# Optimization experiments

Hardware: AMD Instinct MI355X
Metric: run time of the kernel (lower is better)

The kernel has to match this reference:

```python
import jax, jax.numpy as jnp
import numpy as np

N, E, D, ED, SH = 100000, 1600000, 64, 16, 9

# Real spherical harmonics l=0,1,2, 'integral' normalization (e3nn default),
# applied to unit direction vectors. Coefficients: 1/(2*sqrt(pi)), sqrt(3/4pi), etc.

def _sh(d):
    x, y, z = d[:, 0], d[:, 1], d[:, 2]
    return jnp.stack([
        jnp.full_like(x, 0.28209479177387814),          # l=0
        0.4886025119029199 * y,                          # l=1, m=-1
        0.4886025119029199 * z,                          # l=1, m=0
        0.4886025119029199 * x,                          # l=1, m=1
        1.0925484305920792 * x * y,                      # l=2, m=-2
        1.0925484305920792 * y * z,                      # l=2, m=-1
        0.31539156525252005 * (3.0 * z * z - 1.0),       # l=2, m=0
        1.0925484305920792 * x * z,                      # l=2, m=1
        0.5462742152960396 * (x * x - y * y),            # l=2, m=2
    ], axis=1)


def _mlp(h, W1, b1, W2, b2):  # Linear -> SiLU -> Linear
    return jax.nn.silu(h @ W1 + b1) @ W2 + b2


def setup_inputs() -> dict:
    key = jax.random.key(0)
    ks = jax.random.split(key, 16)
    def rn(k, shape, scale=0.05):
        return jax.random.normal(k, shape, dtype=jnp.float32) * scale
    return {
        "x": jax.random.normal(ks[0], (N, D), jnp.float32),
        "pos": jax.random.normal(ks[1], (N, 3), jnp.float32) * 3.0,
        "edge_attr": jax.random.normal(ks[2], (E, ED), jnp.float32),
        "row": jax.random.randint(ks[3], (E,), 0, N, dtype=jnp.int32),
        "col": jax.random.randint(ks[4], (E,), 0, N, dtype=jnp.int32),
        "node_W1": rn(ks[5], (D, D)), "node_b1": jnp.zeros((D,), jnp.float32),
        "node_W2": rn(ks[6], (D, D)), "node_b2": jnp.zeros((D,), jnp.float32),
        "edge_W1": rn(ks[7], (SH + ED, D)), "edge_b1": jnp.zeros((D,), jnp.float32),
        "edge_W2": rn(ks[8], (D, D)), "edge_b2": jnp.zeros((D,), jnp.float32),
        "out_W1": rn(ks[9], (2 * D, D)), "out_b1": jnp.zeros((D,), jnp.float32),
        "out_W2": rn(ks[10], (D, D)), "out_b2": jnp.zeros((D,), jnp.float32),
        "bn_gamma": jnp.ones((D,), jnp.float32), "bn_beta": jnp.zeros((D,), jnp.float32),
    }


def reference(x, pos, edge_attr, row, col,
              node_W1, node_b1, node_W2, node_b2,
              edge_W1, edge_b1, edge_W2, edge_b2,
              out_W1, out_b1, out_W2, out_b2,
              bn_gamma, bn_beta):
    # gather node positions per edge -> relative vectors
    rel = pos[row] - pos[col]                                    # [E,3]
    length = jnp.sqrt(jnp.sum(rel * rel, axis=1, keepdims=True) + 1e-12)
    d = rel / length
    d = d / (jnp.sqrt(jnp.sum(d * d, axis=1, keepdims=True)) + 1e-10)
    edge_sh = _sh(d)                                             # [E,9]
    edge_feat = jnp.concatenate([edge_sh, edge_attr], axis=1)    # [E,9+ED]
    x_t = _mlp(x, node_W1, node_b1, node_W2, node_b2)            # [N,D]
    e_w = _mlp(edge_feat, edge_W1, edge_b1, edge_W2, edge_b2)    # [E,D]
    msg = x_t[row] * e_w                                         # message = x_j * edge_attr
    # scatter-mean onto target nodes (edge_index[1] == col)
    s = jax.ops.segment_sum(msg, col, num_segments=N)            # [N,D]
    cnt = jax.ops.segment_sum(jnp.ones((E,), msg.dtype), col, num_segments=N)
    agg = s / jnp.maximum(cnt, 1.0)[:, None]
    h = jnp.concatenate([agg, x], axis=1)                        # [N,2D]
    h = _mlp(h, out_W1, out_b1, out_W2, out_b2)                  # [N,D]
    # BatchNorm over node dim (scalar irreps), training-mode batch stats
    mean = jnp.mean(h, axis=0)
    var = jnp.var(h, axis=0)
    return (h - mean) / jnp.sqrt(var + 1e-5) * bn_gamma + bn_beta
```

## Files before the change

kernel.cpp:

```cpp
#include <hip/hip_runtime.h>
#include <math.h>

#define DD 64
#define EDA 16

#define FR_E1 0
#define FR_E2 4
#define FR_N1 12
#define FR_N2 20
#define FR_O1 28
#define FR_O2 44
#define FR_TOT 52

#define PADH 72
#define PADF 68

#define HS 72
#define PF 68

typedef unsigned int u32;
typedef __attribute__((ext_vector_type(8))) short short8;
typedef __attribute__((ext_vector_type(4))) float f32x4;

static __device__ __forceinline__ float silu(float v) {
    return v / (1.0f + __expf(-v));
}
static __device__ __forceinline__ unsigned short f2bf(float f) {
    unsigned u = __float_as_uint(f);
    unsigned r = u + 0x7FFFu + ((u >> 16) & 1u);
    return (unsigned short)(r >> 16);
}
static __device__ __forceinline__ float bf2f(unsigned short u) {
    return __uint_as_float(((unsigned)u) << 16);
}
static __device__ __forceinline__ unsigned cvt_pk_bf16(float lo, float hi) {
    unsigned r;
    asm("v_cvt_pk_bf16_f32 %0, %1, %2" : "=v"(r) : "v"(lo), "v"(hi));
    return r;
}
static __device__ __forceinline__ int bperm(int idx_lane, int v) {
    return __builtin_amdgcn_ds_bpermute(idx_lane << 2, v);
}
static __device__ __forceinline__ void wave_lds_fence() {
    asm volatile("s_waitcnt lgkmcnt(0)" ::: "memory");
    __builtin_amdgcn_sched_barrier(0);
}

__global__ __launch_bounds__(256) void k_pack_w(
    const float* __restrict__ eW1, const float* __restrict__ eW2,
    const float* __restrict__ nW1, const float* __restrict__ nW2,
    const float* __restrict__ oW1, const float* __restrict__ oW2,
    unsigned short* __restrict__ wpk)
{
    int t = threadIdx.x;
    int nt = t >> 6, l = t & 63;
    int kc = l >> 4, n0 = l & 15;

    #pragma unroll
    for (int j = 0; j < 8; ++j) {
        int k = kc*8 + j;
        int orig = (k < 16) ? (9 + k) : ((k < 25) ? (k - 16) : -1);
        float v = (orig >= 0) ? eW1[orig*DD + nt*16 + n0] : 0.0f;
        wpk[((size_t)((FR_E1 + nt)*64 + l))*8 + j] = f2bf(v);
    }
    #pragma unroll
    for (int s = 0; s < 2; ++s) {
        #pragma unroll
        for (int j = 0; j < 8; ++j) {
            int k = s*32 + kc*8 + j;
            wpk[((size_t)((FR_E2 + s*4 + nt)*64 + l))*8 + j] = f2bf(eW2[k*DD + nt*16 + n0]);
            wpk[((size_t)((FR_N1 + s*4 + nt)*64 + l))*8 + j] = f2bf(nW1[k*DD + nt*16 + n0]);
            wpk[((size_t)((FR_N2 + s*4 + nt)*64 + l))*8 + j] = f2bf(nW2[k*DD + nt*16 + n0]);
            wpk[((size_t)((FR_O2 + s*4 + nt)*64 + l))*8 + j] = f2bf(oW2[k*DD + nt*16 + n0]);
        }
    }
    #pragma unroll
    for (int s = 0; s < 4; ++s) {
        #pragma unroll
        for (int j = 0; j < 8; ++j) {
            int k = s*32 + kc*8 + j;
            wpk[((size_t)((FR_O1 + s*4 + nt)*64 + l))*8 + j] = f2bf(oW1[k*DD + nt*16 + n0]);
        }
    }
}

__global__ __launch_bounds__(256) void k_hist(
    const int* __restrict__ col, u32* __restrict__ cnt, int n_e)
{
    int g = blockIdx.x * 256 + threadIdx.x;
    int base = g * 4;
    if (base + 3 < n_e) {
        int4 c = ((const int4*)col)[g];
        atomicAdd(&cnt[c.x], 1u);
        atomicAdd(&cnt[c.y], 1u);
        atomicAdd(&cnt[c.z], 1u);
        atomicAdd(&cnt[c.w], 1u);
    } else {
        for (int e = base; e < n_e; ++e) atomicAdd(&cnt[col[e]], 1u);
    }
}

__global__ __launch_bounds__(256) void k_scan1(
    const u32* __restrict__ cnt, u32* __restrict__ bsum, int n)
{
    __shared__ u32 s[256];
    int i = blockIdx.x * 256 + threadIdx.x;
    s[threadIdx.x] = (i < n) ? cnt[i] : 0u;
    __syncthreads();
    for (int o = 128; o > 0; o >>= 1) {
        if (threadIdx.x < o) s[threadIdx.x] += s[threadIdx.x + o];
        __syncthreads();
    }
    if (threadIdx.x == 0) bsum[blockIdx.x] = s[0];
}

__global__ __launch_bounds__(512) void k_scan2(
    const u32* __restrict__ bsum, u32* __restrict__ boff, int nb)
{
    __shared__ u32 s[512];
    int t = threadIdx.x;
    u32 v = (t < nb) ? bsum[t] : 0u;
    s[t] = v;
    __syncthreads();
    for (int o = 1; o < 512; o <<= 1) {
        u32 a = (t >= o) ? s[t - o] : 0u;
        __syncthreads();
        s[t] += a;
        __syncthreads();
    }
    if (t < nb) boff[t] = s[t] - v;
}

__global__ __launch_bounds__(256) void k_scan3(
    const u32* __restrict__ cnt, const u32* __restrict__ boff,
    u32* __restrict__ wp, int n)
{
    __shared__ u32 s[256];
    int t = threadIdx.x;
    int i = blockIdx.x * 256 + t;
    u32 v = (i < n) ? cnt[i] : 0u;
    s[t] = v;
    __syncthreads();
    for (int o = 1; o < 256; o <<= 1) {
        u32 a = (t >= o) ? s[t - o] : 0u;
        __syncthreads();
        s[t] += a;
        __syncthreads();
    }
    if (i < n) wp[i] = boff[blockIdx.x] + s[t] - v;
}

__global__ __launch_bounds__(256) void k_scatter(
    const int* __restrict__ row, const int* __restrict__ col,
    u32* __restrict__ wp, uint2* __restrict__ ce, int n_e)
{
    int e = blockIdx.x * 256 + threadIdx.x;
    if (e >= n_e) return;
    int c = col[e];
    int r = row[e];
    u32 p = atomicAdd(&wp[c], 1u);
    uint2 pk;
    pk.x = (u32)e | ((u32)r << 21);
    pk.y = ((u32)r >> 11) | ((u32)c << 6);
    ce[p] = pk;
}

__global__ __launch_bounds__(256, 2) void k_node_mfma(
    const float* __restrict__ x,
    const unsigned short* __restrict__ wpk,
    const float* __restrict__ b1, const float* __restrict__ b2,
    unsigned short* __restrict__ x_tb, int n)
{
    __shared__ __align__(16) unsigned short tile[4][16*PADH];
    const int tid  = threadIdx.x;
    const int wv   = tid >> 6;
    const int lane = tid & 63;
    const int kc   = lane >> 4;
    const int n0   = lane & 15;
    const int rbase = kc * 4;

    const short8* fb = (const short8*)wpk;
    short8 bw1[2][4], bw2[2][4];
    #pragma unroll
    for (int s = 0; s < 2; ++s)
        #pragma unroll
        for (int nt = 0; nt < 4; ++nt) {
            bw1[s][nt] = fb[(FR_N1 + s*4 + nt)*64 + lane];
            bw2[s][nt] = fb[(FR_N2 + s*4 + nt)*64 + lane];
        }
    float b1v[4], b2v[4];
    #pragma unroll
    for (int nt = 0; nt < 4; ++nt) { b1v[nt] = b1[nt*16 + n0]; b2v[nt] = b2[nt*16 + n0]; }

    const int base = blockIdx.x*64 + wv*16;
    int rc = min(base + n0, n - 1);
    const float* xr = x + (size_t)rc * DD;

    short8 a[2];
    #pragma unroll
    for (int m = 0; m < 2; ++m) {
        float4 u0 = *(const float4*)(xr + m*32 + kc*8);
        float4 u1 = *(const float4*)(xr + m*32 + kc*8 + 4);
        unsigned* au = (unsigned*)&a[m];
        au[0] = cvt_pk_bf16(u0.x, u0.y);
        au[1] = cvt_pk_bf16(u0.z, u0.w);
        au[2] = cvt_pk_bf16(u1.x, u1.y);
        au[3] = cvt_pk_bf16(u1.z, u1.w);
    }

    f32x4 zz = {0.f, 0.f, 0.f, 0.f};
    f32x4 hacc[4] = {zz, zz, zz, zz};
    #pragma unroll
    for (int m = 0; m < 2; ++m)
        #pragma unroll
        for (int nt = 0; nt < 4; ++nt)
            hacc[nt] = __builtin_amdgcn_mfma_f32_16x16x32_bf16(a[m], bw1[m][nt], hacc[nt], 0, 0, 0);

    #pragma unroll
    for (int nt = 0; nt < 4; ++nt)
        #pragma unroll
        for (int r = 0; r < 4; ++r)
            tile[wv][(rbase + r)*PADH + nt*16 + n0] = f2bf(silu(hacc[nt][r] + b1v[nt]));
    __syncthreads();

    short8 a2_0 = *(const short8*)&tile[wv][n0*PADH +  0 + kc*8];
    short8 a2_1 = *(const short8*)&tile[wv][n0*PADH + 32 + kc*8];
    f32x4 oacc[4];
    #pragma unroll
    for (int nt = 0; nt < 4; ++nt) {
        oacc[nt] = __builtin_amdgcn_mfma_f32_16x16x32_bf16(a2_0, bw2[0][nt], zz, 0, 0, 0);
        oacc[nt] = __builtin_amdgcn_mfma_f32_16x16x32_bf16(a2_1, bw2[1][nt], oacc[nt], 0, 0, 0);
    }
    __syncthreads();

    #pragma unroll
    for (int nt = 0; nt < 4; ++nt)
        #pragma unroll
        for (int r = 0; r < 4; ++r)
            tile[wv][(rbase + r)*PADH + nt*16 + n0] = f2bf(oacc[nt][r] + b2v[nt]);
    __syncthreads();

    int ei = lane >> 2, q = lane & 3;
    int er = base + ei;
    if (er < n) {
        uint4* dst = (uint4*)(x_tb + (size_t)er * DD);
        dst[q]     = *(const uint4*)&tile[wv][ei*PADH + q*8];
        dst[q + 4] = *(const uint4*)&tile[wv][ei*PADH + (q + 4)*8];
    }
}

__global__ __launch_bounds__(256, 3) void k_edge_fused(
    const float* __restrict__ pos,
    const float* __restrict__ edge_attr,
    const uint2* __restrict__ ce,
    const unsigned short* __restrict__ x_tb,
    const unsigned short* __restrict__ wpk,
    const float* __restrict__ b1, const float* __restrict__ b2,
    float* __restrict__ agg, int n_e)
{
    __shared__ __align__(16) unsigned short hid_s[4][16*HS];
    __shared__ __align__(16) float          msg_s[4][16*PF];

    const int tid  = threadIdx.x;
    const int wv   = tid >> 6;
    const int lane = tid & 63;
    const int kc   = lane >> 4;
    const int n0   = lane & 15;

    const short8* fb = (const short8*)wpk;
    short8 bw1[4], bw2[2][4];
    #pragma unroll
    for (int nt = 0; nt < 4; ++nt) bw1[nt] = fb[(FR_E1 + nt)*64 + lane];
    #pragma unroll
    for (int s = 0; s < 2; ++s)
        #pragma unroll
        for (int nt = 0; nt < 4; ++nt) bw2[s][nt] = fb[(FR_E2 + s*4 + nt)*64 + lane];

    float4 b1q[4], b2q[4];
    #pragma unroll
    for (int nt = 0; nt < 4; ++nt) {
        b1q[nt] = *(const float4*)(b1 + nt*16 + kc*4);
        b2q[nt] = *(const float4*)(b2 + nt*16 + kc*4);
    }

    const int gbase = blockIdx.x*256 + wv*64;
    int g  = gbase + lane;
    int gc = min(g, n_e - 1);
    uint2 pk = ce[gc];
    int eo = (int)(pk.x & 0x1FFFFFu);
    int rw = (int)((pk.x >> 21) | ((pk.y & 0x3Fu) << 11));
    int cl = (int)(pk.y >> 6);

    float ax = pos[3*rw+0] - pos[3*cl+0];
    float ay = pos[3*rw+1] - pos[3*cl+1];
    float az = pos[3*rw+2] - pos[3*cl+2];
    float len = sqrtf(fmaf(ax,ax, fmaf(ay,ay, az*az)) + 1e-12f);
    float dx = ax/len, dy = ay/len, dz = az/len;
    float n2 = sqrtf(fmaf(dx,dx, fmaf(dy,dy, dz*dz)));
    float inv = 1.0f/(n2 + 1e-10f);
    dx *= inv; dy *= inv; dz *= inv;

    u32 shp01 = cvt_pk_bf16(0.28209479177387814f, 0.4886025119029199f*dy);
    u32 shp23 = cvt_pk_bf16(0.4886025119029199f*dz, 0.4886025119029199f*dx);
    u32 shp45 = cvt_pk_bf16(1.0925484305920792f*dx*dy, 1.0925484305920792f*dy*dz);
    u32 shp67 = cvt_pk_bf16(0.31539156525252005f*(3.0f*dz*dz - 1.0f),
                            1.0925484305920792f*dx*dz);
    u32 shp8  = cvt_pk_bf16(0.5462742152960396f*(dx*dx - dy*dy), 0.0f);

    f32x4 zz = {0.f, 0.f, 0.f, 0.f};

    #pragma unroll 1
    for (int t = 0; t < 4; ++t) {
        const int le = t*16 + n0;
        bool valid = (gbase + le) < n_e;

        int ea  = bperm(le, eo);
        int rv  = bperm(le, rw);
        u32 s01 = (u32)bperm(le, (int)shp01);
        u32 s23 = (u32)bperm(le, (int)shp23);
        u32 s45 = (u32)bperm(le, (int)shp45);
        u32 s67 = (u32)bperm(le, (int)shp67);
        u32 s8  = (u32)bperm(le, (int)shp8);

        const unsigned short* xrow = x_tb + (size_t)rv * DD;
        uint2 xv0 = *(const uint2*)(xrow +  0 + kc*4);
        uint2 xv1 = *(const uint2*)(xrow + 16 + kc*4);
        uint2 xv2 = *(const uint2*)(xrow + 32 + kc*4);
        uint2 xv3 = *(const uint2*)(xrow + 48 + kc*4);
        if (!valid) {
            xv0.x = xv0.y = xv1.x = xv1.y = 0u;
            xv2.x = xv2.y = xv3.x = xv3.y = 0u;
        }

        short8 af;
        unsigned* au = (unsigned*)&af;
        if (kc < 2) {
            const float4* ap = (const float4*)(edge_attr + (size_t)ea*EDA + kc*8);
            float4 a0 = ap[0], a1 = ap[1];
            au[0] = cvt_pk_bf16(a0.x, a0.y);
            au[1] = cvt_pk_bf16(a0.z, a0.w);
            au[2] = cvt_pk_bf16(a1.x, a1.y);
            au[3] = cvt_pk_bf16(a1.z, a1.w);
        } else if (kc == 2) {
            au[0] = s01; au[1] = s23; au[2] = s45; au[3] = s67;
        } else {
            au[0] = s8; au[1] = 0u; au[2] = 0u; au[3] = 0u;
        }

        f32x4 hacc[4];
        #pragma unroll
        for (int nt = 0; nt < 4; ++nt)
            hacc[nt] = __builtin_amdgcn_mfma_f32_16x16x32_bf16(bw1[nt], af, zz, 0, 0, 0);

        #pragma unroll
        for (int nt = 0; nt < 4; ++nt) {
            float h0 = silu(hacc[nt][0] + b1q[nt].x);
            float h1 = silu(hacc[nt][1] + b1q[nt].y);
            float h2 = silu(hacc[nt][2] + b1q[nt].z);
            float h3 = silu(hacc[nt][3] + b1q[nt].w);
            uint2 pr;
            pr.x = cvt_pk_bf16(h0, h1);
            pr.y = cvt_pk_bf16(h2, h3);
            *(uint2*)&hid_s[wv][n0*HS + nt*16 + kc*4] = pr;
        }
        wave_lds_fence();

        short8 bf0 = *(const short8*)&hid_s[wv][n0*HS +  0 + kc*8];
        short8 bf1 = *(const short8*)&hid_s[wv][n0*HS + 32 + kc*8];
        f32x4 oacc[4];
        #pragma unroll
        for (int nt = 0; nt < 4; ++nt) {
            oacc[nt] = __builtin_amdgcn_mfma_f32_16x16x32_bf16(bw2[0][nt], bf0, zz, 0, 0, 0);
            oacc[nt] = __builtin_amdgcn_mfma_f32_16x16x32_bf16(bw2[1][nt], bf1, oacc[nt], 0, 0, 0);
        }

        {
            float4 m;
            m.x = (oacc[0][0] + b2q[0].x) * bf2f((unsigned short)(xv0.x));
            m.y = (oacc[0][1] + b2q[0].y) * bf2f((unsigned short)(xv0.x >> 16));
            m.z = (oacc[0][2] + b2q[0].z) * bf2f((unsigned short)(xv0.y));
            m.w = (oacc[0][3] + b2q[0].w) * bf2f((unsigned short)(xv0.y >> 16));
            *(float4*)&msg_s[wv][n0*PF +  0 + kc*4] = m;
            m.x = (oacc[1][0] + b2q[1].x) * bf2f((unsigned short)(xv1.x));
            m.y = (oacc[1][1] + b2q[1].y) * bf2f((unsigned short)(xv1.x >> 16));
            m.z = (oacc[1][2] + b2q[1].z) * bf2f((unsigned short)(xv1.y));
            m.w = (oacc[1][3] + b2q[1].w) * bf2f((unsigned short)(xv1.y >> 16));
            *(float4*)&msg_s[wv][n0*PF + 16 + kc*4] = m;
            m.x = (oacc[2][0] + b2q[2].x) * bf2f((unsigned short)(xv2.x));
            m.y = (oacc[2][1] + b2q[2].y) * bf2f((unsigned short)(xv2.x >> 16));
            m.z = (oacc[2][2] + b2q[2].z) * bf2f((unsigned short)(xv2.y));
            m.w = (oacc[2][3] + b2q[2].w) * bf2f((unsigned short)(xv2.y >> 16));
            *(float4*)&msg_s[wv][n0*PF + 32 + kc*4] = m;
            m.x = (oacc[3][0] + b2q[3].x) * bf2f((unsigned short)(xv3.x));
            m.y = (oacc[3][1] + b2q[3].y) * bf2f((unsigned short)(xv3.x >> 16));
            m.z = (oacc[3][2] + b2q[3].z) * bf2f((unsigned short)(xv3.y));
            m.w = (oacc[3][3] + b2q[3].w) * bf2f((unsigned short)(xv3.y >> 16));
            *(float4*)&msg_s[wv][n0*PF + 48 + kc*4] = m;
        }
        wave_lds_fence();

        {
            float acc = 0.0f;
            int cur = __builtin_amdgcn_readlane(cl, t*16 + 0);
            #pragma unroll
            for (int r = 0; r < 16; ++r) {
                acc += msg_s[wv][r*PF + lane];
                int nxt = (r < 15) ? __builtin_amdgcn_readlane(cl, t*16 + r + 1) : -1;
                if (nxt != cur) {
                    unsafeAtomicAdd(&agg[(size_t)cur*DD + lane], acc);
                    acc = 0.0f;
                    cur = nxt;
                }
            }
        }
    }
}

__global__ __launch_bounds__(256, 2) void k_out_mfma(
    const float* __restrict__ agg, const u32* __restrict__ cnt,
    const float* __restrict__ x,
    const unsigned short* __restrict__ wpk,
    const float* __restrict__ b1, const float* __restrict__ b2,
    float* __restrict__ h, float* __restrict__ sums, int n)
{
    __shared__ __align__(16) unsigned short htile[4][16*PADH];
    __shared__ __align__(16) float otile[4][16*PADF];
    const int tid  = threadIdx.x;
    const int wv   = tid >> 6;
    const int lane = tid & 63;
    const int kc   = lane >> 4;
    const int n0   = lane & 15;
    const int rbase = kc * 4;

    const short8* fb = (const short8*)wpk;
    short8 bw1[4][4], bw2[2][4];
    #pragma unroll
    for (int s = 0; s < 4; ++s)
        #pragma unroll
        for (int nt = 0; nt < 4; ++nt) bw1[s][nt] = fb[(FR_O1 + s*4 + nt)*64 + lane];
    #pragma unroll
    for (int s = 0; s < 2; ++s)
        #pragma unroll
        for (int nt = 0; nt < 4; ++nt) bw2[s][nt] = fb[(FR_O2 + s*4 + nt)*64 + lane];

    float b1v[4], b2v[4];
    #pragma unroll
    for (int nt = 0; nt < 4; ++nt) { b1v[nt] = b1[nt*16 + n0]; b2v[nt] = b2[nt*16 + n0]; }

    const int base = blockIdx.x*64 + wv*16;
    int rc = min(base + n0, n - 1);
    const float* ar = agg + (size_t)rc * DD;
    const float* xr = x   + (size_t)rc * DD;
    float invc = 1.0f / fmaxf((float)cnt[rc], 1.0f);

    short8 a[4];
    #pragma unroll
    for (int m = 0; m < 4; ++m) {
        const float* src = (m < 2) ? (ar + m*32 + kc*8) : (xr + (m-2)*32 + kc*8);
        float4 u0 = *(const float4*)(src);
        float4 u1 = *(const float4*)(src + 4);
        if (m < 2) {
            u0.x*=invc; u0.y*=invc; u0.z*=invc; u0.w*=invc;
            u1.x*=invc; u1.y*=invc; u1.z*=invc; u1.w*=invc;
        }
        unsigned* au = (unsigned*)&a[m];
        au[0] = cvt_pk_bf16(u0.x, u0.y);
        au[1] = cvt_pk_bf16(u0.z, u0.w);
        au[2] = cvt_pk_bf16(u1.x, u1.y);
        au[3] = cvt_pk_bf16(u1.z, u1.w);
    }

    f32x4 zz = {0.f, 0.f, 0.f, 0.f};
    f32x4 hacc[4] = {zz, zz, zz, zz};
    #pragma unroll
    for (int m = 0; m < 4; ++m)
        #pragma unroll
        for (int nt = 0; nt < 4; ++nt)
            hacc[nt] = __builtin_amdgcn_mfma_f32_16x16x32_bf16(a[m], bw1[m][nt], hacc[nt], 0, 0, 0);

    #pragma unroll
    for (int nt = 0; nt < 4; ++nt)
        #pragma unroll
        for (int r = 0; r < 4; ++r)
            htile[wv][(rbase + r)*PADH + nt*16 + n0] = f2bf(silu(hacc[nt][r] + b1v[nt]));
    __syncthreads();

    short8 a2_0 = *(const short8*)&htile[wv][n0*PADH +  0 + kc*8];
    short8 a2_1 = *(const short8*)&htile[wv][n0*PADH + 32 + kc*8];
    f32x4 oacc[4];
    #pragma unroll
    for (int nt = 0; nt < 4; ++nt) {
        oacc[nt] = __builtin_amdgcn_mfma_f32_16x16x32_bf16(a2_0, bw2[0][nt], zz, 0, 0, 0);
        oacc[nt] = __builtin_amdgcn_mfma_f32_16x16x32_bf16(a2_1, bw2[1][nt], oacc[nt], 0, 0, 0);
    }

    #pragma unroll
    for (int nt = 0; nt < 4; ++nt)
        #pragma unroll
        for (int r = 0; r < 4; ++r)
            otile[wv][(rbase + r)*PADF + nt*16 + n0] = oacc[nt][r] + b2v[nt];
    __syncthreads();

    int ei = lane >> 2, q = lane & 3;
    int er = base + ei;
    if (er < n) {
        float4* dst = (float4*)(h + (size_t)er * DD);
        #pragma unroll
        for (int k = 0; k < 4; ++k)
            dst[q + 4*k] = *(const float4*)&otile[wv][ei*PADF + (q + 4*k)*4];
    }

    if (tid < 64) {
        int f = tid;
        float s = 0.f, qq = 0.f;
        #pragma unroll
        for (int w = 0; w < 4; ++w) {
            int base_w = blockIdx.x*64 + w*16;
            int nv = n - base_w;
            nv = nv < 0 ? 0 : (nv > 16 ? 16 : nv);
            for (int r = 0; r < nv; ++r) {
                float v = otile[w][r*PADF + f];
                s += v; qq = fmaf(v, v, qq);
            }
        }
        unsafeAtomicAdd(&sums[f], s);
        unsafeAtomicAdd(&sums[DD + f], qq);
    }
}

__global__ void k_bn_finalize(const float* __restrict__ sums,
                              const float* __restrict__ gamma, const float* __restrict__ beta,
                              float* __restrict__ ss, float inv_n)
{
    int j = threadIdx.x;
    float m = sums[j] * inv_n;
    float var = sums[DD+j] * inv_n - m*m;
    float sc = gamma[j] * rsqrtf(var + 1e-5f);
    ss[j] = sc;
    ss[DD+j] = beta[j] - m*sc;
}

__global__ __launch_bounds__(256) void k_bn_norm(
    float* __restrict__ h, const float* __restrict__ ss, int total4)
{
    int g = blockIdx.x*256 + threadIdx.x;
    if (g >= total4) return;
    int f0 = (g*4) & (DD-1);
    float4 v = ((const float4*)h)[g];
    v.x = fmaf(v.x, ss[f0+0], ss[DD+f0+0]);
    v.y = fmaf(v.y, ss[f0+1], ss[DD+f0+1]);
    v.z = fmaf(v.z, ss[f0+2], ss[DD+f0+2]);
    v.w = fmaf(v.w, ss[f0+3], ss[DD+f0+3]);
    ((float4*)h)[g] = v;
}

static inline size_t al16(size_t v) { return (v + 15) & ~(size_t)15; }

extern "C" void kernel_launch(void* const* d_in, const int* in_sizes, int n_in,
                              void* d_out, int out_size, void* d_ws, size_t ws_size,
                              hipStream_t stream)
{
    const float* x         = (const float*)d_in[0];
    const float* pos       = (const float*)d_in[1];
    const float* edge_attr = (const float*)d_in[2];
    const int*   row       = (const int*)d_in[3];
    const int*   col       = (const int*)d_in[4];
    const float* nW1 = (const float*)d_in[5];
    const float* nb1 = (const float*)d_in[6];
    const float* nW2 = (const float*)d_in[7];
    const float* nb2 = (const float*)d_in[8];
    const float* eW1 = (const float*)d_in[9];
    const float* eb1 = (const float*)d_in[10];
    const float* eW2 = (const float*)d_in[11];
    const float* eb2 = (const float*)d_in[12];
    const float* oW1 = (const float*)d_in[13];
    const float* ob1 = (const float*)d_in[14];
    const float* oW2 = (const float*)d_in[15];
    const float* ob2 = (const float*)d_in[16];
    const float* gamma = (const float*)d_in[17];
    const float* beta  = (const float*)d_in[18];

    const int N = in_sizes[0] / DD;
    const int E = in_sizes[3];
    const int NB = (N + 255) / 256;

    float* hout = (float*)d_out;
    char* ws = (char*)d_ws;

    size_t o_xtb  = 0;
    size_t o_cnt  = o_xtb  + (size_t)N*DD*2;
    size_t o_sums = o_cnt  + (size_t)N*4;
    size_t o_agg  = o_sums + 128*4;
    size_t o_ss   = o_agg  + (size_t)N*DD*4;
    size_t o_wp   = o_ss   + 128*4;
    size_t o_bsum = o_wp   + (size_t)N*4;
    size_t o_boff = al16(o_bsum + (size_t)NB*4);
    size_t o_wpk  = al16(o_boff + (size_t)NB*4);
    size_t o_ce   = al16(o_wpk + (size_t)FR_TOT*64*8*2);
    size_t need   = o_ce + (size_t)E*8;

    if (ws_size < need) return;

    unsigned short* x_tb = (unsigned short*)(ws + o_xtb);
    u32*   cnt  = (u32*)(ws + o_cnt);
    float* sums = (float*)(ws + o_sums);
    float* agg  = (float*)(ws + o_agg);
    float* ssb  = (float*)(ws + o_ss);
    u32*   wp   = (u32*)(ws + o_wp);
    u32*   bsum = (u32*)(ws + o_bsum);
    u32*   boff = (u32*)(ws + o_boff);
    unsigned short* wpk = (unsigned short*)(ws + o_wpk);
    uint2* ce   = (uint2*)(ws + o_ce);

    hipMemsetAsync(cnt, 0, (size_t)N*4 + 128*4 + (size_t)N*DD*4, stream);

    k_pack_w<<<1, 256, 0, stream>>>(eW1, eW2, nW1, nW2, oW1, oW2, wpk);
    k_hist <<<(E/4 + 255)/256, 256, 0, stream>>>(col, cnt, E);
    k_scan1<<<NB, 256, 0, stream>>>(cnt, bsum, N);
    k_scan2<<<1, 512, 0, stream>>>(bsum, boff, NB);
    k_scan3<<<NB, 256, 0, stream>>>(cnt, boff, wp, N);
    k_scatter<<<(E + 255)/256, 256, 0, stream>>>(row, col, wp, ce, E);
    k_node_mfma<<<(N + 63)/64, 256, 0, stream>>>(x, wpk, nb1, nb2, x_tb, N);
    k_edge_fused<<<(E + 255)/256, 256, 0, stream>>>(pos, edge_attr, ce, x_tb,
                                                    wpk, eb1, eb2, agg, E);
    k_out_mfma<<<(N + 63)/64, 256, 0, stream>>>(agg, cnt, x, wpk, ob1, ob2, hout, sums, N);
    k_bn_finalize<<<1, 64, 0, stream>>>(sums, gamma, beta, ssb, 1.0f/(float)N);
    k_bn_norm<<<(N*DD/4 + 255)/256, 256, 0, stream>>>(hout, ssb, N*DD/4);
}
```

Measured before the change: 408.7 us.

## Software-pipeline edge gathers two tiles ahead and fold BN finalize into normalize

The edge kernel's four-tile loop is unrolled into an issue/compute pipeline. Gathers for x_tb rows, edge_attr and the permuted SH values for the next tiles are issued before the current tile's MFMA and scatter work, so the gather latency is hidden. Launch bounds go from 3 to 4 blocks per SM, which tightens the register budget even though the two prefetch buffers need more registers, so spilling is a risk. The separate one-block BN finalize kernel is removed: each normalize thread now recomputes mean and scale from the sums, dropping one launch at the cost of redundant rsqrt work.

Result: slower. 517.6 us (+26.6%).

```diff
diff --git a/kernel.cpp b/kernel.cpp
--- a/kernel.cpp
+++ b/kernel.cpp
@@ -249,7 +249,14 @@
     }
 }
 
-__global__ __launch_bounds__(256, 3) void k_edge_fused(
+struct Pf {
+    int ea, rv;
+    float4 a0, a1;
+    uint2 x0, x1, x2, x3;
+    u32 s01, s23, s45, s67, s8;
+};
+
+__global__ __launch_bounds__(256, 4) void k_edge_fused(
     const float* __restrict__ pos,
     const float* __restrict__ edge_attr,
     const uint2* __restrict__ ce,
@@ -309,42 +316,41 @@
 
     f32x4 zz = {0.f, 0.f, 0.f, 0.f};
 
-    #pragma unroll 1
-    for (int t = 0; t < 4; ++t) {
-        const int le = t*16 + n0;
-        bool valid = (gbase + le) < n_e;
-
-        int ea  = bperm(le, eo);
-        int rv  = bperm(le, rw);
-        u32 s01 = (u32)bperm(le, (int)shp01);
-        u32 s23 = (u32)bperm(le, (int)shp23);
-        u32 s45 = (u32)bperm(le, (int)shp45);
-        u32 s67 = (u32)bperm(le, (int)shp67);
-        u32 s8  = (u32)bperm(le, (int)shp8);
-
-        const unsigned short* xrow = x_tb + (size_t)rv * DD;
-        uint2 xv0 = *(const uint2*)(xrow +  0 + kc*4);
-        uint2 xv1 = *(const uint2*)(xrow + 16 + kc*4);
-        uint2 xv2 = *(const uint2*)(xrow + 32 + kc*4);
-        uint2 xv3 = *(const uint2*)(xrow + 48 + kc*4);
-        if (!valid) {
-            xv0.x = xv0.y = xv1.x = xv1.y = 0u;
-            xv2.x = xv2.y = xv3.x = xv3.y = 0u;
-        }
+    auto issue = [&](Pf& P, int tt) {
+        const int le = tt*16 + n0;
+        P.ea  = bperm(le, eo);
+        P.rv  = bperm(le, rw);
+        P.s01 = (u32)bperm(le, (int)shp01);
+        P.s23 = (u32)bperm(le, (int)shp23);
+        P.s45 = (u32)bperm(le, (int)shp45);
+        P.s67 = (u32)bperm(le, (int)shp67);
+        P.s8  = (u32)bperm(le, (int)shp8);
+        if (kc < 2) {
+            const float4* ap = (const float4*)(edge_attr + (size_t)P.ea*EDA + kc*8);
+            P.a0 = ap[0];
+            P.a1 = ap[1];
+        }
+        const unsigned short* xrow = x_tb + (size_t)P.rv * DD;
+        P.x0 = *(const uint2*)(xrow +  0 + kc*4);
+        P.x1 = *(const uint2*)(xrow + 16 + kc*4);
+        P.x2 = *(const uint2*)(xrow + 32 + kc*4);
+        P.x3 = *(const uint2*)(xrow + 48 + kc*4);
+    };
+
+    auto compute = [&](const Pf& P, int tt) {
+        bool valid = (gbase + tt*16 + n0) < n_e;
 
         short8 af;
         unsigned* au = (unsigned*)&af;
         if (kc < 2) {
-            const float4* ap = (const float4*)(edge_attr + (size_t)ea*EDA + kc*8);
-            float4 a0 = ap[0], a1 = ap[1];
-            au[0] = cvt_pk_bf16(a0.x, a0.y);
-            au[1] = cvt_pk_bf16(a0.z, a0.w);
-            au[2] = cvt_pk_bf16(a1.x, a1.y);
-            au[3] = cvt_pk_bf16(a1.z, a1.w);
+            au[0] = cvt_pk_bf16(P.a0.x, P.a0.y);
+            au[1] = cvt_pk_bf16(P.a0.z, P.a0.w);
+            au[2] = cvt_pk_bf16(P.a1.x, P.a1.y);
+            au[3] = cvt_pk_bf16(P.a1.z, P.a1.w);
         } else if (kc == 2) {
-            au[0] = s01; au[1] = s23; au[2] = s45; au[3] = s67;
+            au[0] = P.s01; au[1] = P.s23; au[2] = P.s45; au[3] = P.s67;
         } else {
-            au[0] = s8; au[1] = 0u; au[2] = 0u; au[3] = 0u;
+            au[0] = P.s8; au[1] = 0u; au[2] = 0u; au[3] = 0u;
         }
 
         f32x4 hacc[4];
@@ -374,6 +380,11 @@
             oacc[nt] = __builtin_amdgcn_mfma_f32_16x16x32_bf16(bw2[1][nt], bf1, oacc[nt], 0, 0, 0);
         }
 
+        uint2 xv0 = P.x0, xv1 = P.x1, xv2 = P.x2, xv3 = P.x3;
+        if (!valid) {
+            xv0.x = xv0.y = xv1.x = xv1.y = 0u;
+            xv2.x = xv2.y = xv3.x = xv3.y = 0u;
+        }
         {
             float4 m;
             m.x = (oacc[0][0] + b2q[0].x) * bf2f((unsigned short)(xv0.x));
@@ -401,11 +412,11 @@
 
         {
             float acc = 0.0f;
-            int cur = __builtin_amdgcn_readlane(cl, t*16 + 0);
+            int cur = __builtin_amdgcn_readlane(cl, tt*16 + 0);
             #pragma unroll
             for (int r = 0; r < 16; ++r) {
                 acc += msg_s[wv][r*PF + lane];
-                int nxt = (r < 15) ? __builtin_amdgcn_readlane(cl, t*16 + r + 1) : -1;
+                int nxt = (r < 15) ? __builtin_amdgcn_readlane(cl, tt*16 + r + 1) : -1;
                 if (nxt != cur) {
                     unsafeAtomicAdd(&agg[(size_t)cur*DD + lane], acc);
                     acc = 0.0f;
@@ -413,7 +424,17 @@
                 }
             }
         }
-    }
+    };
+
+    Pf pf0, pf1;
+    issue(pf0, 0);
+    issue(pf1, 1);
+    compute(pf0, 0);
+    issue(pf0, 2);
+    compute(pf1, 1);
+    issue(pf1, 3);
+    compute(pf0, 2);
+    compute(pf1, 3);
 }
 
 __global__ __launch_bounds__(256, 2) void k_out_mfma(
@@ -528,29 +549,28 @@
     }
 }
 
-__global__ void k_bn_finalize(const float* __restrict__ sums,
-                              const float* __restrict__ gamma, const float* __restrict__ beta,
-                              float* __restrict__ ss, float inv_n)
-{
-    int j = threadIdx.x;
-    float m = sums[j] * inv_n;
-    float var = sums[DD+j] * inv_n - m*m;
-    float sc = gamma[j] * rsqrtf(var + 1e-5f);
-    ss[j] = sc;
-    ss[DD+j] = beta[j] - m*sc;
-}
-
 __global__ __launch_bounds__(256) void k_bn_norm(
-    float* __restrict__ h, const float* __restrict__ ss, int total4)
+    float* __restrict__ h, const float* __restrict__ sums,
+    const float* __restrict__ gamma, const float* __restrict__ beta,
+    float inv_n, int total4)
 {
     int g = blockIdx.x*256 + threadIdx.x;
     if (g >= total4) return;
     int f0 = (g*4) & (DD-1);
     float4 v = ((const float4*)h)[g];
-    v.x = fmaf(v.x, ss[f0+0], ss[DD+f0+0]);
-    v.y = fmaf(v.y, ss[f0+1], ss[DD+f0+1]);
-    v.z = fmaf(v.z, ss[f0+2], ss[DD+f0+2]);
-    v.w = fmaf(v.w, ss[f0+3], ss[DD+f0+3]);
+    float4 sm = *(const float4*)(sums + f0);
+    float4 sq = *(const float4*)(sums + DD + f0);
+    float4 gm = *(const float4*)(gamma + f0);
+    float4 bt = *(const float4*)(beta + f0);
+    float m0 = sm.x*inv_n, m1 = sm.y*inv_n, m2 = sm.z*inv_n, m3 = sm.w*inv_n;
+    float s0 = gm.x * rsqrtf(sq.x*inv_n - m0*m0 + 1e-5f);
+    float s1 = gm.y * rsqrtf(sq.y*inv_n - m1*m1 + 1e-5f);
+    float s2 = gm.z * rsqrtf(sq.z*inv_n - m2*m2 + 1e-5f);
+    float s3 = gm.w * rsqrtf(sq.w*inv_n - m3*m3 + 1e-5f);
+    v.x = fmaf(v.x - m0, s0, bt.x);
+    v.y = fmaf(v.y - m1, s1, bt.y);
+    v.z = fmaf(v.z - m2, s2, bt.z);
+    v.w = fmaf(v.w - m3, s3, bt.w);
     ((float4*)h)[g] = v;
 }
 
@@ -591,8 +611,7 @@
     size_t o_cnt  = o_xtb  + (size_t)N*DD*2;
     size_t o_sums = o_cnt  + (size_t)N*4;
     size_t o_agg  = o_sums + 128*4;
-    size_t o_ss   = o_agg  + (size_t)N*DD*4;
-    size_t o_wp   = o_ss   + 128*4;
+    size_t o_wp   = o_agg  + (size_t)N*DD*4;
     size_t o_bsum = o_wp   + (size_t)N*4;
     size_t o_boff = al16(o_bsum + (size_t)NB*4);
     size_t o_wpk  = al16(o_boff + (size_t)NB*4);
@@ -605,7 +624,6 @@
     u32*   cnt  = (u32*)(ws + o_cnt);
     float* sums = (float*)(ws + o_sums);
     float* agg  = (float*)(ws + o_agg);
-    float* ssb  = (float*)(ws + o_ss);
     u32*   wp   = (u32*)(ws + o_wp);
     u32*   bsum = (u32*)(ws + o_bsum);
     u32*   boff = (u32*)(ws + o_boff);
@@ -624,6 +642,6 @@
     k_edge_fused<<<(E + 255)/256, 256, 0, stream>>>(pos, edge_attr, ce, x_tb,
                                                     wpk, eb1, eb2, agg, E);
     k_out_mfma<<<(N + 63)/64, 256, 0, stream>>>(agg, cnt, x, wpk, ob1, ob2, hout, sums, N);
-    k_bn_finalize<<<1, 64, 0, stream>>>(sums, gamma, beta, ssb, 1.0f/(float)N);
-    k_bn_norm<<<(N*DD/4 + 255)/256, 256, 0, stream>>>(hout, ssb, N*DD/4);
-}
+    k_bn_norm<<<(N*DD/4 + 255)/256, 256, 0, stream>>>(hout, sums, gamma, beta,
+                                                      1.0f/(float)N, N*DD/4);
+}
```
